# Performance work log

Measured on AMD Instinct MI355X. Metric: run time of the kernel, lower is better.

Reference implementation:

```python
import jax, jax.numpy as jnp
import numpy as np

B, T, S, D, H, FF = 4, 1024, 1024, 1024, 16, 4096
DH = D // H
NEG = -1e9
EPS = 1e-5


def setup_inputs() -> dict:
    key = jax.random.key(0)
    ks = jax.random.split(key, 20)
    p = 0.02  # param init scale
    inp = {
        "x": jax.random.normal(ks[0], (B, T, D), jnp.float32),
        "encoder_output": jax.random.normal(ks[1], (B, S, D), jnp.float32),
        "src_mask": jnp.ones((B, 1, 1, S), jnp.bool_),
        "tgt_mask": jnp.tril(jnp.ones((1, 1, T, T), jnp.bool_)),  # causal
        # self-attention params
        "d_Wq": jax.random.normal(ks[2], (D, D)) * p, "d_bq": jnp.zeros((D,)),
        "d_Wk": jax.random.normal(ks[3], (D, D)) * p, "d_bk": jnp.zeros((D,)),
        "d_Wv": jax.random.normal(ks[4], (D, D)) * p, "d_bv": jnp.zeros((D,)),
        "d_Wo": jax.random.normal(ks[5], (D, D)) * p, "d_bo": jnp.zeros((D,)),
        # cross-attention params
        "e_Wq": jax.random.normal(ks[6], (D, D)) * p, "e_bq": jnp.zeros((D,)),
        "e_Wk": jax.random.normal(ks[7], (D, D)) * p, "e_bk": jnp.zeros((D,)),
        "e_Wv": jax.random.normal(ks[8], (D, D)) * p, "e_bv": jnp.zeros((D,)),
        "e_Wo": jax.random.normal(ks[9], (D, D)) * p, "e_bo": jnp.zeros((D,)),
        # FFN params
        "ff_W1": jax.random.normal(ks[10], (D, FF)) * p, "ff_b1": jnp.zeros((FF,)),
        "ff_W2": jax.random.normal(ks[11], (FF, D)) * p, "ff_b2": jnp.zeros((D,)),
        # layernorm params
        "ln1_g": jnp.ones((D,)), "ln1_b": jnp.zeros((D,)),
        "ln2_g": jnp.ones((D,)), "ln2_b": jnp.zeros((D,)),
        "ln3_g": jnp.ones((D,)), "ln3_b": jnp.zeros((D,)),
    }
    return inp


def _mha(xq, xkv, Wq, bq, Wk, bk, Wv, bv, Wo, bo, mask):
    b, tq = xq.shape[0], xq.shape[1]
    q = (xq @ Wq + bq).reshape(b, tq, H, DH).transpose(0, 2, 1, 3)
    k = (xkv @ Wk + bk).reshape(b, -1, H, DH).transpose(0, 2, 1, 3)
    v = (xkv @ Wv + bv).reshape(b, -1, H, DH).transpose(0, 2, 1, 3)
    scores = jnp.einsum("bhqd,bhkd->bhqk", q, k) / np.float32(np.sqrt(DH))
    scores = jnp.where(mask, scores, NEG)
    attn = jax.nn.softmax(scores, axis=-1)
    out = jnp.einsum("bhqk,bhkd->bhqd", attn, v)
    out = out.transpose(0, 2, 1, 3).reshape(b, tq, D)
    return out @ Wo + bo


def _ln(x, g, b):
    m = jnp.mean(x, axis=-1, keepdims=True)
    v = jnp.var(x, axis=-1, keepdims=True)
    return (x - m) / jnp.sqrt(v + EPS) * g + b


def reference(x, encoder_output, src_mask, tgt_mask,
              d_Wq, d_bq, d_Wk, d_bk, d_Wv, d_bv, d_Wo, d_bo,
              e_Wq, e_bq, e_Wk, e_bk, e_Wv, e_bv, e_Wo, e_bo,
              ff_W1, ff_b1, ff_W2, ff_b2,
              ln1_g, ln1_b, ln2_g, ln2_b, ln3_g, ln3_b):
    # masked self-attention + residual + LN (dropout is identity in eval)
    d = _mha(x, x, d_Wq, d_bq, d_Wk, d_bk, d_Wv, d_bv, d_Wo, d_bo, tgt_mask)
    d = _ln(d + x, ln1_g, ln1_b)
    # cross-attention over encoder output + residual + LN
    f = _mha(d, encoder_output, e_Wq, e_bq, e_Wk, e_bk, e_Wv, e_bv, e_Wo, e_bo, src_mask)
    f = _ln(f + d, ln2_g, ln2_b)
    # FFN + residual + LN
    g = jax.nn.relu(f @ ff_W1 + ff_b1) @ ff_W2 + ff_b2
    g = _ln(g + f, ln3_g, ln3_b)
    return g
```

## Files before the change

### kernel.cpp

```cpp
#include <hip/hip_runtime.h>

static constexpr int Bc = 4, Tc = 1024, Sc = 1024, Dc = 1024, Hc = 16, DHc = 64, FFc = 4096;

typedef __attribute__((ext_vector_type(8))) short short8;
typedef __attribute__((ext_vector_type(4))) short short4v;
typedef __attribute__((ext_vector_type(4))) float f32x4;

__device__ __forceinline__ unsigned short f2bf(float f) {
    unsigned int u = __float_as_uint(f);
    unsigned int r = u + 0x7fffu + ((u >> 16) & 1u);
    return (unsigned short)(r >> 16);
}
__device__ __forceinline__ float bf2f(unsigned short u) {
    return __uint_as_float(((unsigned int)u) << 16);
}
__device__ __forceinline__ float fexp2(float x) {
    float r; asm("v_exp_f32 %0, %1" : "=v"(r) : "v"(x)); return r;
}
__device__ __forceinline__ unsigned int cvtpk(float a, float b) {
    unsigned int r;
    asm("v_cvt_pk_bf16_f32 %0, %1, %2" : "=v"(r) : "v"(a), "v"(b));
    return r;
}

__device__ __forceinline__ void gload_lds16(const void* g, void* l) {
    __builtin_amdgcn_global_load_lds((const __attribute__((address_space(1))) void*)g,
                                     (__attribute__((address_space(3))) void*)l, 16, 0, 0);
}

__global__ __launch_bounds__(256) void cast_f32_bf16(const float* __restrict__ in,
                                                     unsigned short* __restrict__ out, int n8) {
    int i = blockIdx.x * 256 + threadIdx.x;
    if (i >= n8) return;
    const float4* p = (const float4*)in + (size_t)i * 2;
    float4 a = p[0], b = p[1];
    short8 o;
    o[0] = f2bf(a.x); o[1] = f2bf(a.y); o[2] = f2bf(a.z); o[3] = f2bf(a.w);
    o[4] = f2bf(b.x); o[5] = f2bf(b.y); o[6] = f2bf(b.z); o[7] = f2bf(b.w);
    *(short8*)(out + (size_t)i * 8) = o;
}

__global__ __launch_bounds__(256) void transpose_cast(const float* __restrict__ W,
                                                      unsigned short* __restrict__ Wt,
                                                      int K, int N) {
    __shared__ float tile[32][33];
    int n0 = blockIdx.x * 32, k0 = blockIdx.y * 32;
    int tx = threadIdx.x, ty = threadIdx.y;
#pragma unroll
    for (int i = 0; i < 4; i++)
        tile[ty + i * 8][tx] = W[(size_t)(k0 + ty + i * 8) * N + n0 + tx];
    __syncthreads();
#pragma unroll
    for (int i = 0; i < 4; i++)
        Wt[(size_t)(n0 + ty + i * 8) * K + k0 + tx] = f2bf(tile[tx][ty + i * 8]);
}

struct TP8 { const float* s[8]; unsigned short* d[8]; };
__global__ __launch_bounds__(256) void transpose_cast8(TP8 p) {
    __shared__ float tile[32][33];
    const float* W = p.s[blockIdx.z];
    unsigned short* Wt = p.d[blockIdx.z];
    int n0 = blockIdx.x * 32, k0 = blockIdx.y * 32;
    int tx = threadIdx.x, ty = threadIdx.y;
#pragma unroll
    for (int i = 0; i < 4; i++)
        tile[ty + i * 8][tx] = W[(size_t)(k0 + ty + i * 8) * 1024 + n0 + tx];
    __syncthreads();
#pragma unroll
    for (int i = 0; i < 4; i++)
        Wt[(size_t)(n0 + ty + i * 8) * 1024 + k0 + tx] = f2bf(tile[tx][ty + i * 8]);
}

__global__ void concat_bias(const float* b0, const float* b1, const float* b2,
                            float* __restrict__ out) {
    int i = blockIdx.x * 256 + threadIdx.x;
    int seg = i >> 10, j = i & 1023;
    const float* p = seg == 0 ? b0 : (seg == 1 ? b1 : b2);
    out[i] = p[j];
}

__global__ __launch_bounds__(256) void transpose_v(const unsigned short* __restrict__ V, int ldv,
                                                   unsigned short* __restrict__ Vt) {
    __shared__ unsigned short t[64 * 64];
    const int bh = blockIdx.y, b = bh >> 4, h = bh & 15;
    const int s0 = blockIdx.x * 64;
    const int tid = threadIdx.x;
    const int r = tid >> 2, ch = tid & 3;
    const unsigned short* src = V + (size_t)(b * 1024 + s0 + r) * ldv + h * 64 + ch * 16;
    short8 v0 = *(const short8*)src;
    short8 v1 = *(const short8*)(src + 8);
    int pw_ = (ch ^ r ^ (r >> 4)) & 3;
    *(short8*)(t + r * 64 + pw_ * 16) = v0;
    *(short8*)(t + r * 64 + pw_ * 16 + 8) = v1;
    __syncthreads();
    const int dh = tid >> 2, sc = (tid & 3) * 16;
    short8 o0, o1;
#pragma unroll
    for (int j = 0; j < 8; j++) {
        int c0 = sc + j, c1 = sc + 8 + j;
        o0[j] = t[c0 * 64 + (((dh >> 4) ^ c0 ^ (c0 >> 4)) & 3) * 16 + (dh & 15)];
        o1[j] = t[c1 * 64 + (((dh >> 4) ^ c1 ^ (c1 >> 4)) & 3) * 16 + (dh & 15)];
    }
    unsigned short* dst = Vt + ((size_t)bh * 64 + dh) * 1024 + s0 + sc;
    *(short8*)dst = o0;
    *(short8*)(dst + 8) = o1;
}

struct BlkMap { int m, n, z; };
__device__ __forceinline__ BlkMap remap_block() {
    const int gx = gridDim.x, gy = gridDim.y;
    const int nxy = gx * gy;
    const int nwg = nxy * gridDim.z;
    const int flat = (blockIdx.z * gy + blockIdx.y) * gx + blockIdx.x;
    const int id = (flat & 7) * (nwg >> 3) + (flat >> 3);
    const int pz = id / nxy;
    const int rz = id - pz * nxy;
    const int gwsh = (gx & 7) ? 2 : 3;
    const int gw = 1 << gwsh;
    const int gsz = gw * gy;
    const int grp = rz / gsz;
    const int rem = rz - grp * gsz;
    BlkMap r;
    r.m = rem >> gwsh;
    r.n = (grp << gwsh) + (rem & (gw - 1));
    r.z = pz;
    return r;
}

template <int EPI>
__global__ __launch_bounds__(512, 2) void gemm256(const unsigned short* __restrict__ A,
                                                  const unsigned short* __restrict__ Bt,
                                                  const float* __restrict__ bias,
                                                  unsigned short* __restrict__ outB,
                                                  int N, int lda, int ldb, int nk) {
    __shared__ unsigned short sm[4][16384];
    const int tid = threadIdx.x;
    const int lane = tid & 63, wid = tid >> 6;
    const int l4 = lane & 15, g = lane >> 4;
    const int wr = wid >> 2, wc = wid & 3;
    BlkMap bm = remap_block();
    const int m0 = bm.m * 256, n0 = bm.n * 256, z = bm.z;
    A += (size_t)z * (nk * 64);
    Bt += (size_t)z * (nk * 64);
    const int srow = tid >> 3;
    const int schunk = (tid & 7) ^ (srow & 7);
    const int sw = l4 & 7;

    auto stA = [&](int sb, int seg, int k0) {
        gload_lds16(A + (size_t)(m0 + seg * 64 + srow) * lda + k0 + schunk * 8,
                    (char*)sm[sb] + seg * 8192 + tid * 16);
    };
    auto stB = [&](int sb, int seg, int k0) {
        gload_lds16(Bt + (size_t)(n0 + seg * 64 + srow) * ldb + k0 + schunk * 8,
                    (char*)sm[2 + sb] + seg * 8192 + tid * 16);
    };

    f32x4 acc[8][4] = {};
#pragma unroll
    for (int s = 0; s < 4; s++) stB(0, s, 0);
#pragma unroll
    for (int s = 0; s < 4; s++) stA(0, s, 0);
    asm volatile("s_waitcnt vmcnt(0)" ::: "memory");
    __builtin_amdgcn_s_barrier();

    for (int t = 0; t < nk; ++t) {
        const int bufR = t & 1, bufW = bufR ^ 1;
        const int kn = (t + 1) * 64;
        const bool pf = (t + 1 < nk);
        const unsigned short* As_ = sm[bufR];
        const unsigned short* Bs_ = sm[2 + bufR];
        short8 a[4], b0[4], b1[4];
        if (pf) { stB(bufW, 0, kn); stB(bufW, 1, kn); }
#pragma unroll
        for (int n = 0; n < 4; n++)
            b0[n] = *(const short8*)(Bs_ + (wc * 64 + n * 16 + l4) * 64 + (g ^ sw) * 8);
#pragma unroll
        for (int m = 0; m < 4; m++)
            a[m] = *(const short8*)(As_ + (wr * 128 + m * 16 + l4) * 64 + (g ^ sw) * 8);
        __builtin_amdgcn_s_barrier();
        __builtin_amdgcn_s_setprio(1);
#pragma unroll
        for (int m = 0; m < 4; m++)
#pragma unroll
            for (int n = 0; n < 4; n++)
                acc[m][n] = __builtin_amdgcn_mfma_f32_16x16x32_bf16(a[m], b0[n], acc[m][n], 0, 0, 0);
        __builtin_amdgcn_s_setprio(0);
        __builtin_amdgcn_s_barrier();
        if (pf) { stB(bufW, 2, kn); stB(bufW, 3, kn); }
#pragma unroll
        for (int n = 0; n < 4; n++)
            b1[n] = *(const short8*)(Bs_ + (wc * 64 + n * 16 + l4) * 64 + ((4 + g) ^ sw) * 8);
#pragma unroll
        for (int m = 0; m < 4; m++)
            a[m] = *(const short8*)(As_ + (wr * 128 + m * 16 + l4) * 64 + ((4 + g) ^ sw) * 8);
        __builtin_amdgcn_s_barrier();
        __builtin_amdgcn_s_setprio(1);
#pragma unroll
        for (int m = 0; m < 4; m++)
#pragma unroll
            for (int n = 0; n < 4; n++)
                acc[m][n] = __builtin_amdgcn_mfma_f32_16x16x32_bf16(a[m], b1[n], acc[m][n], 0, 0, 0);
        __builtin_amdgcn_s_setprio(0);
        if (pf) asm volatile("s_waitcnt vmcnt(4)" ::: "memory");
        else    asm volatile("s_waitcnt vmcnt(0)" ::: "memory");
        __builtin_amdgcn_s_barrier();
        if (pf) { stA(bufW, 0, kn); stA(bufW, 2, kn); }
#pragma unroll
        for (int m = 0; m < 4; m++)
            a[m] = *(const short8*)(As_ + (wr * 128 + 64 + m * 16 + l4) * 64 + (g ^ sw) * 8);
        __builtin_amdgcn_s_barrier();
        __builtin_amdgcn_s_setprio(1);
#pragma unroll
        for (int m = 0; m < 4; m++)
#pragma unroll
            for (int n = 0; n < 4; n++)
                acc[4 + m][n] = __builtin_amdgcn_mfma_f32_16x16x32_bf16(a[m], b0[n], acc[4 + m][n], 0, 0, 0);
        __builtin_amdgcn_s_setprio(0);
        __builtin_amdgcn_s_barrier();
        if (pf) { stA(bufW, 1, kn); stA(bufW, 3, kn); }
#pragma unroll
        for (int m = 0; m < 4; m++)
            a[m] = *(const short8*)(As_ + (wr * 128 + 64 + m * 16 + l4) * 64 + ((4 + g) ^ sw) * 8);
        __builtin_amdgcn_s_barrier();
        __builtin_amdgcn_s_setprio(1);
#pragma unroll
        for (int m = 0; m < 4; m++)
#pragma unroll
            for (int n = 0; n < 4; n++)
                acc[4 + m][n] = __builtin_amdgcn_mfma_f32_16x16x32_bf16(a[m], b1[n], acc[4 + m][n], 0, 0, 0);
        __builtin_amdgcn_s_setprio(0);
        if (pf) asm volatile("s_waitcnt vmcnt(2)" ::: "memory");
        __builtin_amdgcn_s_barrier();
    }
    const int rowB = m0 + wr * 128 + g * 4;
    const int colB = n0 + wc * 64 + l4;
    unsigned short* oB = outB;
    if (EPI == 3) oB += (size_t)z * ((size_t)gridDim.y * 256) * N;
#pragma unroll
    for (int n = 0; n < 4; n++) {
        float bv = (EPI == 3 && z != 0) ? 0.f : bias[colB + n * 16];
#pragma unroll
        for (int m = 0; m < 8; m++) {
#pragma unroll
            for (int r = 0; r < 4; r++) {
                float v = acc[m][n][r] + bv;
                if (EPI == 2) v = fmaxf(v, 0.f);
                oB[(size_t)(rowB + m * 16 + r) * N + colB + n * 16] = f2bf(v);
            }
        }
    }
}

template <int EPI>
__global__ __launch_bounds__(256) void gemm64_db(const unsigned short* __restrict__ A,
                                                 const unsigned short* __restrict__ Bt,
                                                 const float* __restrict__ bias,
                                                 float* __restrict__ outF,
                                                 unsigned short* __restrict__ outB,
                                                 int M, int N, int Kloop, int lda, int ldb) {
    __shared__ unsigned short As[3][64 * 32];
    __shared__ unsigned short Bs[3][128 * 32];
    const int tid = threadIdx.x;
    const int w = tid >> 6, lane = tid & 63, l4 = lane & 15, g = lane >> 4;
    BlkMap bm = remap_block();
    const int m0 = bm.m * 64, n0 = bm.n * 128;
    f32x4 acc[4][2] = {};
    const int r0 = tid >> 2;
    const int kk = ((tid & 3) ^ ((tid >> 3) & 3)) * 8;
    const int sk = (l4 >> 1) & 3;
    const unsigned short* Ar0 = A + (size_t)(m0 + r0) * lda + kk;
    const unsigned short* Br0 = Bt + (size_t)(n0 + r0) * ldb + kk;
    const unsigned short* Br1 = Bt + (size_t)(n0 + 64 + r0) * ldb + kk;
    auto stage = [&](int sb, int k0) {
        gload_lds16(Ar0 + k0, (char*)As[sb] + tid * 16);
        gload_lds16(Br0 + k0, (char*)Bs[sb] + tid * 16);
        gload_lds16(Br1 + k0, (char*)Bs[sb] + 4096 + tid * 16);
    };
    const int nk = Kloop >> 5;
    stage(0, 0);
    stage(1, 32);
    asm volatile("s_waitcnt vmcnt(3)" ::: "memory");
    __builtin_amdgcn_s_barrier();
    asm volatile("" ::: "memory");
    int buf = 0;
    for (int t = 0; t < nk; ++t) {
        if (t + 2 < nk) {
            int b2 = buf + 2; if (b2 >= 3) b2 -= 3;
            stage(b2, (t + 2) * 32);
        }
        short8 a[4], b[2];
#pragma unroll
        for (int m = 0; m < 4; m++)
            a[m] = *(const short8*)(As[buf] + (m * 16 + l4) * 32 + (g ^ sk) * 8);
#pragma unroll
        for (int n = 0; n < 2; n++)
            b[n] = *(const short8*)(Bs[buf] + (w * 32 + n * 16 + l4) * 32 + (g ^ sk) * 8);
#pragma unroll
        for (int m = 0; m < 4; m++)
#pragma unroll
            for (int n = 0; n < 2; n++)
                acc[m][n] = __builtin_amdgcn_mfma_f32_16x16x32_bf16(a[m], b[n], acc[m][n], 0, 0, 0);
        if (t + 1 < nk) {
            if (t + 2 < nk) asm volatile("s_waitcnt vmcnt(3)" ::: "memory");
            else            asm volatile("s_waitcnt vmcnt(0)" ::: "memory");
            __builtin_amdgcn_s_barrier();
            asm volatile("" ::: "memory");
        }
        buf = (buf + 1 == 3) ? 0 : buf + 1;
    }
    const int rowB = m0 + g * 4;
    const int colB = n0 + w * 32 + l4;
#pragma unroll
    for (int n = 0; n < 2; n++) {
        float bv = bias[colB + n * 16];
#pragma unroll
        for (int m = 0; m < 4; m++) {
#pragma unroll
            for (int r = 0; r < 4; r++) {
                float v = acc[m][n][r] + bv;
                if (EPI == 2) v = fmaxf(v, 0.f);
                size_t idx = (size_t)(rowB + m * 16 + r) * N + colB + n * 16;
                if (EPI == 1) outF[idx] = v;
                else outB[idx] = f2bf(v);
            }
        }
    }
}

template <int CAUSAL>
__global__ __launch_bounds__(256) void attn5_kernel(const unsigned short* __restrict__ Q, int ldq,
                                                    const unsigned short* __restrict__ Kg, int ldk,
                                                    const unsigned short* __restrict__ Vt,
                                                    unsigned short* __restrict__ O) {
    __shared__ unsigned short Kl[2 * 64 * 64];
    __shared__ unsigned short Vl[2 * 64 * 64];
    __shared__ unsigned short Pl[4][16 * 72];
    const int bh = blockIdx.x, qb = blockIdx.y;
    const int b = bh >> 4, h = bh & 15;
    const int tid = threadIdx.x, w = tid >> 6, lane = tid & 63;
    const int l4 = lane & 15, g = lane >> 4;
    const int q0 = qb * 64 + w * 16;
    const unsigned short* Qp = Q + (size_t)(b * Tc + q0 + l4) * ldq + h * DHc + g * 8;
    short8 qf0 = *(const short8*)Qp;
    short8 qf1 = *(const short8*)(Qp + 32);
    const unsigned short* Kbase = Kg + (size_t)(b * 1024) * ldk + h * DHc;
    const unsigned short* Vbase = Vt + (size_t)bh * DHc * 1024;
    f32x4 o[4] = {};
    float mrun = -1e30f, lrun = 0.f;
    const int nT = CAUSAL ? qb + 1 : 16;
    unsigned short* pw = &Pl[w][l4 * 72];
    const int qi = q0 + l4;
    constexpr float SC = 0.125f * 1.44269504f;

    short8 ones;
#pragma unroll
    for (int j = 0; j < 8; j++) ones[j] = (short)0x3F80;

    const int sr0 = tid >> 3;
    const int sr1 = 32 + sr0;
    const int sc_ = (tid & 7) ^ (sr0 & 7);

    auto stage = [&](int s0, int buf) {
        char* kd = (char*)Kl + buf * 8192;
        char* vd = (char*)Vl + buf * 8192;
        gload_lds16(Kbase + (size_t)(s0 + sr0) * ldk + sc_ * 8, kd + tid * 16);
        gload_lds16(Kbase + (size_t)(s0 + sr1) * ldk + sc_ * 8, kd + 4096 + tid * 16);
        gload_lds16(Vbase + (size_t)sr0 * 1024 + s0 + sc_ * 8, vd + tid * 16);
        gload_lds16(Vbase + (size_t)sr1 * 1024 + s0 + sc_ * 8, vd + 4096 + tid * 16);
    };

    stage(0, 0);
    __syncthreads();
    int buf = 0;
    const int sw = l4 & 7;

    for (int t = 0; t < nT; ++t) {
        const int s0 = t * 64;
        if (t + 1 < nT) stage(s0 + 64, buf ^ 1);
        const unsigned short* Kb_ = Kl + buf * 4096;
        const unsigned short* Vb_ = Vl + buf * 4096;
        f32x4 st[4];
        f32x4 z = {0.f, 0.f, 0.f, 0.f};
        __builtin_amdgcn_s_setprio(1);
#pragma unroll
        for (int c = 0; c < 4; c++) {
            const unsigned short* kr = Kb_ + (c * 16 + l4) * 64;
            short8 ka0 = *(const short8*)(kr + ((g ^ sw) * 8));
            short8 ka1 = *(const short8*)(kr + (((g + 4) ^ sw) * 8));
            st[c] = __builtin_amdgcn_mfma_f32_16x16x32_bf16(ka0, qf0, z, 0, 0, 0);
            st[c] = __builtin_amdgcn_mfma_f32_16x16x32_bf16(ka1, qf1, st[c], 0, 0, 0);
        }
        __builtin_amdgcn_s_setprio(0);
        float p[16];
        const bool domask = CAUSAL && (t == nT - 1);
#pragma unroll
        for (int c = 0; c < 4; c++)
#pragma unroll
            for (int r = 0; r < 4; r++) {
                float v = st[c][r] * SC;
                if (domask && (s0 + c * 16 + g * 4 + r) > qi) v = -1e9f;
                p[c * 4 + r] = v;
            }
        float m1 = fmaxf(fmaxf(p[0], p[1]), p[2]);
        float m2 = fmaxf(fmaxf(p[3], p[4]), p[5]);
        float m3 = fmaxf(fmaxf(p[6], p[7]), p[8]);
        float m4 = fmaxf(fmaxf(p[9], p[10]), p[11]);
        float m5 = fmaxf(fmaxf(p[12], p[13]), p[14]);
        float tmax = fmaxf(fmaxf(fmaxf(m1, m2), fmaxf(m3, m4)), fmaxf(m5, p[15]));
        tmax = fmaxf(tmax, __shfl_xor(tmax, 16));
        tmax = fmaxf(tmax, __shfl_xor(tmax, 32));
        if (!__all(tmax <= mrun + 11.5f)) {
            float mnew = fmaxf(mrun, tmax);
            float al = fexp2(mrun - mnew);
            lrun *= al;
#pragma unroll
            for (int d = 0; d < 4; d++) o[d] *= al;
            mrun = mnew;
        }
#pragma unroll
        for (int i = 0; i < 16; i++) p[i] = fexp2(p[i] - mrun);
#pragma unroll
        for (int c = 0; c < 4; c++) {
            uint2 u;
            u.x = cvtpk(p[c * 4 + 0], p[c * 4 + 1]);
            u.y = cvtpk(p[c * 4 + 2], p[c * 4 + 3]);
            *(uint2*)(pw + c * 16 + g * 4) = u;
        }
        short8 pb_lo = *(const short8*)(pw + g * 8);
        short8 pb_hi = *(const short8*)(pw + 32 + g * 8);
        __builtin_amdgcn_s_setprio(1);
        f32x4 s4 = __builtin_amdgcn_mfma_f32_16x16x32_bf16(ones, pb_lo, z, 0, 0, 0);
        s4 = __builtin_amdgcn_mfma_f32_16x16x32_bf16(ones, pb_hi, s4, 0, 0, 0);
#pragma unroll
        for (int d = 0; d < 4; d++) {
            const unsigned short* vr = Vb_ + (d * 16 + l4) * 64;
            short8 va0 = *(const short8*)(vr + ((g ^ sw) * 8));
            short8 va1 = *(const short8*)(vr + (((g + 4) ^ sw) * 8));
            o[d] = __builtin_amdgcn_mfma_f32_16x16x32_bf16(va0, pb_lo, o[d], 0, 0, 0);
            o[d] = __builtin_amdgcn_mfma_f32_16x16x32_bf16(va1, pb_hi, o[d], 0, 0, 0);
        }
        __builtin_amdgcn_s_setprio(0);
        lrun += s4[0];
        __syncthreads();
        buf ^= 1;
    }
    float inv = 1.f / lrun;
    unsigned short* Ob = O + (size_t)(b * Tc + q0 + l4) * Dc + h * DHc;
#pragma unroll
    for (int d = 0; d < 4; d++) {
#pragma unroll
        for (int r = 0; r < 4; r++) Ob[d * 16 + g * 4 + r] = f2bf(o[d][r] * inv);
    }
}

__global__ __launch_bounds__(256) void ln_bf(const unsigned short* __restrict__ a,
                                             const unsigned short* __restrict__ res,
                                             const float* __restrict__ gam,
                                             const float* __restrict__ bet,
                                             unsigned short* __restrict__ outB,
                                             float* __restrict__ outF) {
    int row = blockIdx.x, t = threadIdx.x;
    size_t base = (size_t)row * Dc + t * 4;
    short4v av = *(const short4v*)(a + base);
    short4v rv = *(const short4v*)(res + base);
    float x0 = bf2f((unsigned short)av[0]) + bf2f((unsigned short)rv[0]);
    float x1 = bf2f((unsigned short)av[1]) + bf2f((unsigned short)rv[1]);
    float x2 = bf2f((unsigned short)av[2]) + bf2f((unsigned short)rv[2]);
    float x3 = bf2f((unsigned short)av[3]) + bf2f((unsigned short)rv[3]);
    float s = x0 + x1 + x2 + x3;
    float ss = x0 * x0 + x1 * x1 + x2 * x2 + x3 * x3;
    for (int o = 1; o < 64; o <<= 1) { s += __shfl_xor(s, o); ss += __shfl_xor(ss, o); }
    __shared__ float S1[4], S2[4];
    int w = t >> 6;
    if ((t & 63) == 0) { S1[w] = s; S2[w] = ss; }
    __syncthreads();
    s = S1[0] + S1[1] + S1[2] + S1[3];
    ss = S2[0] + S2[1] + S2[2] + S2[3];
    float mean = s * (1.f / Dc);
    float var = ss * (1.f / Dc) - mean * mean;
    float rstd = rsqrtf(var + 1e-5f);
    int c = t * 4;
    float4 g4 = *(const float4*)(gam + c);
    float4 b4 = *(const float4*)(bet + c);
    float y0 = (x0 - mean) * rstd * g4.x + b4.x;
    float y1 = (x1 - mean) * rstd * g4.y + b4.y;
    float y2 = (x2 - mean) * rstd * g4.z + b4.z;
    float y3 = (x3 - mean) * rstd * g4.w + b4.w;
    if (outB) {
        short4v ob;
        ob[0] = f2bf(y0); ob[1] = f2bf(y1); ob[2] = f2bf(y2); ob[3] = f2bf(y3);
        *(short4v*)(outB + base) = ob;
    }
    if (outF) { float4 ov = {y0, y1, y2, y3}; *(float4*)(outF + base) = ov; }
}

__global__ __launch_bounds__(256) void ln_4b(const unsigned short* __restrict__ p,
                                             const unsigned short* __restrict__ res,
                                             const float* __restrict__ gam,
                                             const float* __restrict__ bet,
                                             float* __restrict__ outF) {
    const size_t PS = (size_t)4096 * 1024;
    int row = blockIdx.x, t = threadIdx.x;
    size_t base = (size_t)row * Dc + t * 4;
    float x0, x1, x2, x3;
    {
        short4v rv = *(const short4v*)(res + base);
        x0 = bf2f((unsigned short)rv[0]); x1 = bf2f((unsigned short)rv[1]);
        x2 = bf2f((unsigned short)rv[2]); x3 = bf2f((unsigned short)rv[3]);
    }
#pragma unroll
    for (int j = 0; j < 4; j++) {
        short4v v = *(const short4v*)(p + j * PS + base);
        x0 += bf2f((unsigned short)v[0]); x1 += bf2f((unsigned short)v[1]);
        x2 += bf2f((unsigned short)v[2]); x3 += bf2f((unsigned short)v[3]);
    }
    float s = x0 + x1 + x2 + x3;
    float ss = x0 * x0 + x1 * x1 + x2 * x2 + x3 * x3;
    for (int o = 1; o < 64; o <<= 1) { s += __shfl_xor(s, o); ss += __shfl_xor(ss, o); }
    __shared__ float S1[4], S2[4];
    int w = t >> 6;
    if ((t & 63) == 0) { S1[w] = s; S2[w] = ss; }
    __syncthreads();
    s = S1[0] + S1[1] + S1[2] + S1[3];
    ss = S2[0] + S2[1] + S2[2] + S2[3];
    float mean = s * (1.f / Dc);
    float var = ss * (1.f / Dc) - mean * mean;
    float rstd = rsqrtf(var + 1e-5f);
    int c = t * 4;
    float4 g4 = *(const float4*)(gam + c);
    float4 b4 = *(const float4*)(bet + c);
    float4 ov;
    ov.x = (x0 - mean) * rstd * g4.x + b4.x;
    ov.y = (x1 - mean) * rstd * g4.y + b4.y;
    ov.z = (x2 - mean) * rstd * g4.z + b4.z;
    ov.w = (x3 - mean) * rstd * g4.w + b4.w;
    *(float4*)(outF + base) = ov;
}

extern "C" void kernel_launch(void* const* d_in, const int* in_sizes, int n_in,
                              void* d_out, int out_size, void* d_ws, size_t ws_size,
                              hipStream_t stream) {
    const float* x   = (const float*)d_in[0];
    const float* enc = (const float*)d_in[1];
    const float* dWq = (const float*)d_in[4];  const float* dbq = (const float*)d_in[5];
    const float* dWk = (const float*)d_in[6];  const float* dbk = (const float*)d_in[7];
    const float* dWv = (const float*)d_in[8];  const float* dbv = (const float*)d_in[9];
    const float* dWo = (const float*)d_in[10]; const float* dbo = (const float*)d_in[11];
    const float* eWq = (const float*)d_in[12]; const float* ebq = (const float*)d_in[13];
    const float* eWk = (const float*)d_in[14]; const float* ebk = (const float*)d_in[15];
    const float* eWv = (const float*)d_in[16]; const float* ebv = (const float*)d_in[17];
    const float* eWo = (const float*)d_in[18]; const float* ebo = (const float*)d_in[19];
    const float* fW1 = (const float*)d_in[20]; const float* fb1 = (const float*)d_in[21];
    const float* fW2 = (const float*)d_in[22]; const float* fb2 = (const float*)d_in[23];
    const float* g1 = (const float*)d_in[24];  const float* be1 = (const float*)d_in[25];
    const float* g2 = (const float*)d_in[26];  const float* be2 = (const float*)d_in[27];
    const float* g3 = (const float*)d_in[28];  const float* be3 = (const float*)d_in[29];

    char* ws = (char*)d_ws;
    size_t off = 0;
    auto alloc = [&](size_t bytes) -> void* {
        void* p = ws + off;
        off += (bytes + 255) & ~(size_t)255;
        return p;
    };
    const size_t A = (size_t)4096 * 1024;
    const size_t MB1 = (size_t)1024 * 1024;
    char* R1 = (char*)alloc(32 * 1024 * 1024);
    unsigned short* qkv = (unsigned short*)R1;
    unsigned short* kvx = (unsigned short*)R1;
    unsigned short* qx  = (unsigned short*)(R1 + 16 * 1024 * 1024);
    unsigned short* h1  = (unsigned short*)R1;
    unsigned short* xb   = (unsigned short*)alloc(A * 2);
    unsigned short* encb = (unsigned short*)alloc(A * 2);
    unsigned short* wqkv = (unsigned short*)alloc(3 * MB1 * 2);
    unsigned short* wekv = (unsigned short*)alloc(2 * MB1 * 2);
    unsigned short* weq  = (unsigned short*)alloc(MB1 * 2);
    unsigned short* wdo  = (unsigned short*)alloc(MB1 * 2);
    unsigned short* weo  = (unsigned short*)alloc(MB1 * 2);
    unsigned short* wf1  = (unsigned short*)alloc(4 * MB1 * 2);
    unsigned short* wf2  = (unsigned short*)alloc(4 * MB1 * 2);
    float* bqkv = (float*)alloc(3072 * 4);
    float* bekv = (float*)alloc(2048 * 4);
    unsigned short* VtB = (unsigned short*)alloc(A * 2);
    unsigned short* ab  = (unsigned short*)alloc(A * 2);
    unsigned short* tmpB = (unsigned short*)alloc(A * 2);
    unsigned short* dB = (unsigned short*)alloc(A * 2);
    unsigned short* fB = (unsigned short*)alloc(A * 2);
    unsigned short* pfb = VtB;
    (void)ws_size; (void)in_sizes; (void)n_in; (void)out_size;

    dim3 tb(32, 8);
    cast_f32_bf16<<<2048, 256, 0, stream>>>(x, xb, (int)(A / 8));
    cast_f32_bf16<<<2048, 256, 0, stream>>>(enc, encb, (int)(A / 8));
    TP8 tp;
    tp.s[0] = dWq; tp.d[0] = wqkv;
    tp.s[1] = dWk; tp.d[1] = wqkv + MB1;
    tp.s[2] = dWv; tp.d[2] = wqkv + 2 * MB1;
    tp.s[3] = eWk; tp.d[3] = wekv;
    tp.s[4] = eWv; tp.d[4] = wekv + MB1;
    tp.s[5] = eWq; tp.d[5] = weq;
    tp.s[6] = dWo; tp.d[6] = wdo;
    tp.s[7] = eWo; tp.d[7] = weo;
    transpose_cast8<<<dim3(32, 32, 8), tb, 0, stream>>>(tp);
    transpose_cast<<<dim3(128, 32), tb, 0, stream>>>(fW1, wf1, 1024, 4096);
    transpose_cast<<<dim3(32, 128), tb, 0, stream>>>(fW2, wf2, 4096, 1024);
    concat_bias<<<12, 256, 0, stream>>>(dbq, dbk, dbv, bqkv);
    concat_bias<<<8, 256, 0, stream>>>(ebk, ebv, ebv, bekv);

    gemm256<0><<<dim3(12, 16), 512, 0, stream>>>(xb, wqkv, bqkv, qkv, 3072, 1024, 1024, 16);
    transpose_v<<<dim3(16, 64), 256, 0, stream>>>(qkv + 2048, 3072, VtB);
    attn5_kernel<1><<<dim3(64, 16), 256, 0, stream>>>(qkv, 3072, qkv + 1024, 3072, VtB, ab);
    gemm64_db<0><<<dim3(8, 64), 256, 0, stream>>>(ab, wdo, dbo, nullptr, tmpB, 4096, 1024, 1024, 1024, 1024);
    ln_bf<<<4096, 256, 0, stream>>>(tmpB, xb, g1, be1, dB, nullptr);

    gemm256<0><<<dim3(8, 16), 512, 0, stream>>>(encb, wekv, bekv, kvx, 2048, 1024, 1024, 16);
    gemm64_db<0><<<dim3(8, 64), 256, 0, stream>>>(dB, weq, ebq, nullptr, qx, 4096, 1024, 1024, 1024, 1024);
    transpose_v<<<dim3(16, 64), 256, 0, stream>>>(kvx + 1024, 2048, VtB);
    attn5_kernel<0><<<dim3(64, 16), 256, 0, stream>>>(qx, 1024, kvx, 2048, VtB, ab);
    gemm64_db<0><<<dim3(8, 64), 256, 0, stream>>>(ab, weo, ebo, nullptr, tmpB, 4096, 1024, 1024, 1024, 1024);
    ln_bf<<<4096, 256, 0, stream>>>(tmpB, dB, g2, be2, fB, nullptr);

    gemm256<2><<<dim3(16, 16), 512, 0, stream>>>(fB, wf1, fb1, h1, 4096, 1024, 1024, 16);
    gemm256<3><<<dim3(4, 16, 4), 512, 0, stream>>>(h1, wf2, fb2, pfb, 1024, 4096, 4096, 16);
    ln_4b<<<4096, 256, 0, stream>>>(pfb, fB, g3, be3, (float*)d_out);
}
```

Baseline: 357.3 us.

## Stage GEMM epilogue through LDS for coalesced stores; reverse causal attention block order

New measurement: 349.2 us. -2.3%, faster.

```diff
diff --git a/kernel.cpp b/kernel.cpp
--- a/kernel.cpp
+++ b/kernel.cpp
@@ -232,22 +232,39 @@
         if (pf) asm volatile("s_waitcnt vmcnt(2)" ::: "memory");
         __builtin_amdgcn_s_barrier();
     }
-    const int rowB = m0 + wr * 128 + g * 4;
-    const int colB = n0 + wc * 64 + l4;
+    unsigned short* eb = (unsigned short*)sm;
     unsigned short* oB = outB;
     if (EPI == 3) oB += (size_t)z * ((size_t)gridDim.y * 256) * N;
-#pragma unroll
-    for (int n = 0; n < 4; n++) {
-        float bv = (EPI == 3 && z != 0) ? 0.f : bias[colB + n * 16];
-#pragma unroll
-        for (int m = 0; m < 8; m++) {
-#pragma unroll
-            for (int r = 0; r < 4; r++) {
-                float v = acc[m][n][r] + bv;
-                if (EPI == 2) v = fmaxf(v, 0.f);
-                oB[(size_t)(rowB + m * 16 + r) * N + colB + n * 16] = f2bf(v);
+    const int colL = wc * 64 + l4;
+#pragma unroll
+    for (int h = 0; h < 2; ++h) {
+        if (wr == h) {
+#pragma unroll
+            for (int mm = 0; mm < 8; mm++) {
+                const int base_r = (mm < 4 ? mm * 16 : 64 + (mm - 4) * 16) + g * 4;
+#pragma unroll
+                for (int n = 0; n < 4; n++) {
+                    float bv = (EPI == 3 && z != 0) ? 0.f : bias[n0 + colL + n * 16];
+#pragma unroll
+                    for (int r = 0; r < 4; r++) {
+                        float v = acc[mm][n][r] + bv;
+                        if (EPI == 2) v = fmaxf(v, 0.f);
+                        eb[(base_r + r) * 260 + colL + n * 16] = f2bf(v);
+                    }
+                }
             }
         }
+        __syncthreads();
+        const int gr0 = m0 + h * 128;
+#pragma unroll
+        for (int j = 0; j < 8; j++) {
+            const int f = j * 8192 + tid * 16;
+            const int row = f >> 9;
+            const int colb = f & 511;
+            short8 v = *(const short8*)((const char*)eb + row * 520 + colb);
+            *(short8*)(oB + (size_t)(gr0 + row) * N + n0 + (colb >> 1)) = v;
+        }
+        if (h == 0) __syncthreads();
     }
 }
 
@@ -335,7 +352,8 @@
     __shared__ unsigned short Kl[2 * 64 * 64];
     __shared__ unsigned short Vl[2 * 64 * 64];
     __shared__ unsigned short Pl[4][16 * 72];
-    const int bh = blockIdx.x, qb = blockIdx.y;
+    const int bh = blockIdx.x;
+    const int qb = CAUSAL ? (gridDim.y - 1 - blockIdx.y) : blockIdx.y;
     const int b = bh >> 4, h = bh & 15;
     const int tid = threadIdx.x, w = tid >> 6, lane = tid & 63;
     const int l4 = lane & 15, g = lane >> 4;
```
